# Optimization experiments

Hardware: AMD Instinct MI355X
Metric: run time of the kernel (lower is better)

## Reference

```python
import jax, jax.numpy as jnp
import numpy as np

B, S, D = 2, 2048, 768
C = 8                # num_channels
R = D // C           # ternary_rank = 96 (RoPE head_dim)
THETA = 10000.0
TERNARY_STD = 0.2
TERNARY_SCALE = 1.0  # ternary_factor_scaling


def _rope_tables():
    # HF-style RoPE: inv_freq over half dim, emb = concat(freqs, freqs)
    inv_freq = 1.0 / (THETA ** (np.arange(0, R, 2, dtype=np.float32) / R))
    pos = np.arange(S, dtype=np.float32)
    freqs = pos[:, None] * inv_freq[None, :]          # [S, R/2]
    emb = np.concatenate([freqs, freqs], axis=-1)     # [S, R]
    cos = np.broadcast_to(np.cos(emb)[None], (B, S, R)).copy()
    sin = np.broadcast_to(np.sin(emb)[None], (B, S, R)).copy()
    return jnp.asarray(cos), jnp.asarray(sin)


def setup_inputs() -> dict:
    key = jax.random.key(0)
    k1, k2, k3 = jax.random.split(key, 3)
    qz = jax.random.normal(k1, (B, S, D), dtype=jnp.float32)
    U = jax.random.normal(k2, (D, D), dtype=jnp.float32) * TERNARY_STD
    V = jax.random.normal(k3, (D, D), dtype=jnp.float32) * TERNARY_STD
    cos, sin = _rope_tables()
    return {"qz": qz, "cos": cos, "sin": sin, "U": U, "V": V}


def _rotate_half(x):
    h = x.shape[-1] // 2
    return jnp.concatenate([-x[..., h:], x[..., :h]], axis=-1)


def reference(qz, cos, sin, U, V):
    # cos/sin: [B,S,R] -> broadcast over channel dim -> [B,1,S,R]
    cosb = cos[:, None, :, :]
    sinb = sin[:, None, :, :]
    rope = lambda x: x * cosb + _rotate_half(x) * sinb       # apply
    rope_o = lambda x: x * cosb - _rotate_half(x) * sinb     # apply_o (inverse)

    # projections: F.linear(qz, W) == qz @ W.T
    qz_u = (qz @ U.T * TERNARY_SCALE).reshape(B, S, C, R).transpose(0, 2, 1, 3)
    qz_v = (qz @ V.T * TERNARY_SCALE).reshape(B, S, C, R).transpose(0, 2, 1, 3)

    qz_uo = rope_o(qz_u)
    qz_ur = rope(qz_u)
    qz_vr = rope(qz_v)

    # message_F: [B,C,S,S]
    message_F = jnp.einsum('bcqr,bckr->bcqk', qz_ur, qz_vr)
    # softmax(message_F / regularize_h) with regularize_h = 1/D  ->  * D
    qh = jax.nn.softmax((message_F * jnp.float32(D)).astype(jnp.float32), axis=-1).astype(qz_ur.dtype)

    qh_v1 = rope_o(jnp.einsum('bcqk,bckr->bcqr', qh, qz_vr))  # qh @ qz_v
    qh_v2 = rope(jnp.einsum('bckq,bckr->bcqr', qh, qz_uo))    # qh^T @ qz_uo

    qh_v1 = qh_v1.transpose(0, 2, 1, 3).reshape(B, S, D)
    qh_v2 = qh_v2.transpose(0, 2, 1, 3).reshape(B, S, D)

    message_G = (qh_v1 @ U + qh_v2 @ V) * TERNARY_SCALE
    return message_G
```

## Files before the change

### kernel.cpp

```cpp
#include <hip/hip_runtime.h>

typedef _Float16 f16;
typedef _Float16 f16x8 __attribute__((ext_vector_type(8)));
typedef _Float16 f16x4 __attribute__((ext_vector_type(4)));
typedef float f32x4 __attribute__((ext_vector_type(4)));

#define MFMA16(A,B,C) __builtin_amdgcn_mfma_f32_16x16x32_f16(A,B,C,0,0,0)
#define INV2048 4.8828125e-4f
#define HN (16ll*2048*96)
#define UVN 589824
#define ZC1 1107.98979f
#define ZC2 0.54101064f

__device__ __forceinline__ void split_f16(float x, f16& h, f16& l) {
    h = (f16)x;
    l = (f16)((x - (float)h) * 2048.0f);
}

__global__ __launch_bounds__(256) void k0_split(const float* __restrict__ qz,
                                                const float* __restrict__ U,
                                                const float* __restrict__ V,
                                                f16* __restrict__ qzh, f16* __restrict__ qzl,
                                                f16* __restrict__ Uh, f16* __restrict__ Ul,
                                                f16* __restrict__ Vh, f16* __restrict__ Vl) {
// ... 20 lines not shown
        float4 y = *(const float4*)(V + (size_t)i4 * 4);
        split_f16(y.x, h0, l0); split_f16(y.y, h1, l1);
        split_f16(y.z, h2, l2); split_f16(y.w, h3, l3);
        f16x4 hv2 = {h0, h1, h2, h3};
        f16x4 lv2 = {l0, l1, l2, l3};
        *(f16x4*)(Vh + (size_t)i4 * 4) = hv2;
        *(f16x4*)(Vl + (size_t)i4 * 4) = lv2;
    }
}

__global__ __launch_bounds__(256, 2) void k1_proj(const f16* __restrict__ qzh,
                                                  const f16* __restrict__ qzl,
                                                  const f16* __restrict__ Uh,
                                                  const f16* __restrict__ Ul,
                                                  const f16* __restrict__ Vh,
                                                  const f16* __restrict__ Vl,
                                                  const float* __restrict__ cosb,
                                                  const float* __restrict__ sinb,
                                                  f16* __restrict__ uhp, f16* __restrict__ ulp,
                                                  f16* __restrict__ vhp, f16* __restrict__ vlp,
                                                  f16* __restrict__ vT, f16* __restrict__ oT) {
    __shared__ __align__(16) f16 smem[36864];
    f16* sAh  = smem;
    f16* sAl  = smem + 4608;
    f16* sBuh = smem + 9216;
    f16* sBul = smem + 9216 + 6912;
    f16* sBvh = smem + 9216 + 2 * 6912;
    f16* sBvl = smem + 9216 + 3 * 6912;

    const int tid = threadIdx.x;
    const int w = tid >> 6, lane = tid & 63;
    const int quad = lane >> 4, l15 = lane & 15;
    const int wr = w >> 1, wc = w & 1;
    const int bid0 = blockIdx.y * 64 + blockIdx.x;
    const int swz  = (bid0 & 7) * 64 + (bid0 >> 3);
    const int bs0 = (swz & 63) * 64;
    const int c = swz >> 6;

    const f16* Ug_h = Uh + (size_t)c * 96 * 768;
    const f16* Ug_l = Ul + (size_t)c * 96 * 768;
    const f16* Vg_h = Vh + (size_t)c * 96 * 768;
    const f16* Vg_l = Vl + (size_t)c * 96 * 768;

    f32x4 aUS[2][3] = {}, aUX[2][3] = {};
    f32x4 aVS[2][3] = {}, aVX[2][3] = {};

    for (int k0 = 0; k0 < 768; k0 += 64) {
        __syncthreads();
#pragma unroll
        for (int m = 0; m < 2; ++m) {
            int f = tid + 256 * m, row = f >> 3, cg = f & 7;
            const size_t go = (size_t)(bs0 + row) * 768 + k0 + cg * 8;
            const int lo = row * 72 + cg * 8;
            *(float4*)&sAh[lo] = *(const float4*)(qzh + go);
            *(float4*)&sAl[lo] = *(const float4*)(qzl + go);
        }
#pragma unroll
        for (int m = 0; m < 3; ++m) {
            int f = tid + 256 * m, row = f >> 3, cg = f & 7;
            const size_t go = (size_t)row * 768 + k0 + cg * 8;
            const int lo = row * 72 + cg * 8;
            *(float4*)&sBuh[lo] = *(const float4*)(Ug_h + go);
            *(float4*)&sBul[lo] = *(const float4*)(Ug_l + go);
            *(float4*)&sBvh[lo] = *(const float4*)(Vg_h + go);
            *(float4*)&sBvl[lo] = *(const float4*)(Vg_l + go);
        }
        __syncthreads();
#pragma unroll
        for (int cc = 0; cc < 2; ++cc) {
            f16x8 ah[2], al[2];
#pragma unroll
            for (int mt = 0; mt < 2; ++mt) {
                const int ar = (32 * wr + 16 * mt + l15) * 72 + cc * 32 + quad * 8;
                ah[mt] = *(const f16x8*)&sAh[ar];
                al[mt] = *(const f16x8*)&sAl[ar];
            }
#pragma unroll
            for (int nt = 0; nt < 3; ++nt) {
                const int br = (48 * wc + 16 * nt + l15) * 72 + cc * 32 + quad * 8;
                f16x8 buh = *(const f16x8*)&sBuh[br];
                f16x8 bul = *(const f16x8*)&sBul[br];
                f16x8 bvh = *(const f16x8*)&sBvh[br];
                f16x8 bvl = *(const f16x8*)&sBvl[br];
#pragma unroll
                for (int mt = 0; mt < 2; ++mt) {
                    aUS[mt][nt] = MFMA16(ah[mt], buh, aUS[mt][nt]);
                    aUX[mt][nt] = MFMA16(ah[mt], bul, aUX[mt][nt]);
                    aUX[mt][nt] = MFMA16(al[mt], buh, aUX[mt][nt]);
                    aVS[mt][nt] = MFMA16(ah[mt], bvh, aVS[mt][nt]);
                    aVX[mt][nt] = MFMA16(ah[mt], bvl, aVX[mt][nt]);
                    aVX[mt][nt] = MFMA16(al[mt], bvh, aVX[mt][nt]);
                }
            }
        }
    }

    __syncthreads();
    float* LU = (float*)smem;
    float* LV = LU + 6400;
#pragma unroll
    for (int mt = 0; mt < 2; ++mt)
#pragma unroll
        for (int nt = 0; nt < 3; ++nt)
#pragma unroll
            for (int r = 0; r < 4; ++r) {
                const int sl = 32 * wr + 16 * mt + 4 * quad + r;
                const int col = 48 * wc + 16 * nt + l15;
                LU[sl * 100 + col] = aUS[mt][nt][r] + aUX[mt][nt][r] * INV2048;
                LV[sl * 100 + col] = aVS[mt][nt][r] + aVX[mt][nt][r] * INV2048;
            }
    __syncthreads();

    const int b = bs0 >> 11;
    const int s0 = bs0 & 2047;
    const int head = b * 8 + c;
    const size_t nb = (size_t)head * 2048 * 96;
    const size_t tb = (size_t)head * 96 * 2048;
    const int ty = tid >> 4, tx = tid & 15;

#pragma unroll
    for (int jj = 0; jj < 3; ++jj) {
        int r = tx + 16 * jj;
        f16 vt1[4], vt2[4], ot1[4], ot2[4];
#pragma unroll
        for (int ii = 0; ii < 4; ++ii) {
            int sl = 4 * ty + ii;
            int s = s0 + sl;
            int cbi = (b * 2048 + s) * 96 + r;
            float cc = cosb[cbi], ss = sinb[cbi];
            size_t rowb = nb + (size_t)s * 96;
            float u1 = LU[sl * 100 + r], u2 = LU[sl * 100 + r + 48];
            float v1 = LV[sl * 100 + r], v2 = LV[sl * 100 + r + 48];
            float ur1 = u1 * cc - u2 * ss, ur2 = u2 * cc + u1 * ss;
            float uo1 = u1 * cc + u2 * ss, uo2 = u2 * cc - u1 * ss;
            float vr1 = v1 * cc - v2 * ss, vr2 = v2 * cc + v1 * ss;
            f16 h, l;
            split_f16(ur1, h, l); uhp[rowb + r] = h;      ulp[rowb + r] = l;
            split_f16(ur2, h, l); uhp[rowb + r + 48] = h; ulp[rowb + r + 48] = l;
            split_f16(vr1, h, l); vhp[rowb + r] = h;      vlp[rowb + r] = l;      vt1[ii] = h;
            split_f16(vr2, h, l); vhp[rowb + r + 48] = h; vlp[rowb + r + 48] = l; vt2[ii] = h;
            ot1[ii] = (f16)uo1; ot2[ii] = (f16)uo2;
        }
        f16x4 pv1 = {vt1[0], vt1[1], vt1[2], vt1[3]};
        f16x4 pv2 = {vt2[0], vt2[1], vt2[2], vt2[3]};
        f16x4 po1 = {ot1[0], ot1[1], ot1[2], ot1[3]};
        f16x4 po2 = {ot2[0], ot2[1], ot2[2], ot2[3]};
        *(f16x4*)&vT[tb + (size_t)r * 2048 + s0 + 4 * ty] = pv1;
        *(f16x4*)&vT[tb + (size_t)(r + 48) * 2048 + s0 + 4 * ty] = pv2;
        *(f16x4*)&oT[tb + (size_t)r * 2048 + s0 + 4 * ty] = po1;
        *(f16x4*)&oT[tb + (size_t)(r + 48) * 2048 + s0 + 4 * ty] = po2;
    }
}

__global__ __launch_bounds__(256, 2) void k2_stats(const f16* __restrict__ uhp,
                                                   const f16* __restrict__ ulp,
                                                   const f16* __restrict__ vhp,
                                                   const f16* __restrict__ vlp,
                                                   float* __restrict__ Mo) {
    __shared__ float Mbuf[4][64];
    const int tid = threadIdx.x, w = tid >> 6, lane = tid & 63;
    const int quad = lane >> 4, l15 = lane & 15;
    const int bid0 = blockIdx.y * 32 + blockIdx.x;
    const int swz  = (bid0 & 7) * 64 + (bid0 >> 3);
    const int q0 = (swz & 31) * 64, head = swz >> 5;
    const f16* Ah_g = uhp + (size_t)head * 2048 * 96;
    const f16* Al_g = ulp + (size_t)head * 2048 * 96;

    f16x8 Afh[4][3], Afl[4][3];
#pragma unroll
    for (int mt = 0; mt < 4; ++mt)
#pragma unroll
        for (int cc = 0; cc < 3; ++cc) {
            size_t off = (size_t)(q0 + 16 * mt + l15) * 96 + cc * 32 + quad * 8;
            Afh[mt][cc] = *(const f16x8*)(Ah_g + off);
            Afl[mt][cc] = *(const f16x8*)(Al_g + off);
        }

    const f16* Bh_p = vhp + (size_t)head * 2048 * 96 + (size_t)(w * 16 + l15) * 96 + quad * 8;
    const f16* Bl_p = vlp + (size_t)head * 2048 * 96 + (size_t)(w * 16 + l15) * 96 + quad * 8;

    f16x8 Bch[2][3], Bcl[2][3];
#pragma unroll
    for (int cc = 0; cc < 3; ++cc) {
        Bch[0][cc] = *(const f16x8*)(Bh_p + cc * 32);
        Bcl[0][cc] = *(const f16x8*)(Bl_p + cc * 32);
    }

    float m_run[4][4];
#pragma unroll
    for (int mt = 0; mt < 4; ++mt)
#pragma unroll
        for (int r = 0; r < 4; ++r) m_run[mt][r] = -3.0e38f;

    for (int tp = 0; tp < 16; ++tp) {
#pragma unroll
        for (int h = 0; h < 2; ++h) {
            const int t = 2 * tp + h;
            if (t < 31) {
                const f16* bh = Bh_p + (size_t)(t + 1) * 6144;
                const f16* bl = Bl_p + (size_t)(t + 1) * 6144;
#pragma unroll
                for (int cc = 0; cc < 3; ++cc) {
                    Bch[h ^ 1][cc] = *(const f16x8*)(bh + cc * 32);
                    Bcl[h ^ 1][cc] = *(const f16x8*)(bl + cc * 32);
                }
            }
            f32x4 accS[4] = {}, accX[4] = {};
            __builtin_amdgcn_s_setprio(1);
#pragma unroll
            for (int cc = 0; cc < 3; ++cc)
#pragma unroll
                for (int mt = 0; mt < 4; ++mt) {
                    accS[mt] = MFMA16(Afh[mt][cc], Bch[h][cc], accS[mt]);
                    accX[mt] = MFMA16(Afh[mt][cc], Bcl[h][cc], accX[mt]);
                    accX[mt] = MFMA16(Afl[mt][cc], Bch[h][cc], accX[mt]);
                }
            __builtin_amdgcn_s_setprio(0);
#pragma unroll
            for (int mt = 0; mt < 4; ++mt)
#pragma unroll
                for (int r = 0; r < 4; ++r) {
                    float zl = fmaf(ZC1, accS[mt][r], ZC2 * accX[mt][r]);
                    m_run[mt][r] = fmaxf(m_run[mt][r], zl);
                }
        }
    }
#pragma unroll
    for (int mt = 0; mt < 4; ++mt)
#pragma unroll
        for (int r = 0; r < 4; ++r) {
            float m = m_run[mt][r];
            m = fmaxf(m, __shfl_xor(m, 1)); m = fmaxf(m, __shfl_xor(m, 2));
            m = fmaxf(m, __shfl_xor(m, 4)); m = fmaxf(m, __shfl_xor(m, 8));
            m_run[mt][r] = m;
        }
    if (l15 == 0) {
#pragma unroll
        for (int mt = 0; mt < 4; ++mt)
#pragma unroll
            for (int r = 0; r < 4; ++r)
                Mbuf[w][16 * mt + 4 * quad + r] = m_run[mt][r];
    }
    __syncthreads();
    if (tid < 64) {
        float M = -3.0e38f;
#pragma unroll
        for (int ww = 0; ww < 4; ++ww) M = fmaxf(M, Mbuf[ww][tid]);
        Mo[head * 2048 + q0 + tid] = M;
    }
}

__global__ __launch_bounds__(256, 2) void k3a(const f16* __restrict__ uhp,
                                              const f16* __restrict__ ulp,
                                              const f16* __restrict__ vhp,
                                              const f16* __restrict__ vlp,
                                              const f16* __restrict__ vT,
                                              const float* __restrict__ Mo,
                                              float* __restrict__ Lo,
                                              const float* __restrict__ cosb,
                                              const float* __restrict__ sinb,
                                              f16* __restrict__ w1) {
    __shared__ f16 Vt[2][112 * 72];
    __shared__ f16 P[2][64 * 72];
    const int tid = threadIdx.x, w = tid >> 6, lane = tid & 63;
    const int quad = lane >> 4, l15 = lane & 15;
    const int bid0 = blockIdx.y * 32 + blockIdx.x;
    const int swz  = (bid0 & 7) * 64 + (bid0 >> 3);
    const int q0 = (swz & 31) * 64, head = swz >> 5;
    const f16* Ah_g = uhp + (size_t)head * 2048 * 96;
    const f16* Al_g = ulp + (size_t)head * 2048 * 96;
    const f16* Vt_g = vT + (size_t)head * 96 * 2048;

    f16x8 Afh[4][3], Afl[4][3];
#pragma unroll
    for (int mt = 0; mt < 4; ++mt)
#pragma unroll
        for (int cc = 0; cc < 3; ++cc) {
            size_t off = (size_t)(q0 + 16 * mt + l15) * 96 + cc * 32 + quad * 8;
            Afh[mt][cc] = *(const f16x8*)(Ah_g + off);
            Afl[mt][cc] = *(const f16x8*)(Al_g + off);
        }
    float negM[4][4];
#pragma unroll
    for (int mt = 0; mt < 4; ++mt)
#pragma unroll
        for (int r = 0; r < 4; ++r)
            negM[mt][r] = -Mo[head * 2048 + q0 + 16 * mt + 4 * quad + r];

    const f16* Bh_p = vhp + (size_t)head * 2048 * 96 + (size_t)(w * 16 + l15) * 96 + quad * 8;
    const f16* Bl_p = vlp + (size_t)head * 2048 * 96 + (size_t)(w * 16 + l15) * 96 + quad * 8;
    const int vr0 = tid >> 3, vc8 = (tid & 7) * 8;
    const int pwc = (w * 16 + l15 + 16 * quad) & 63;
    const int prr = 16 * (l15 >> 2);

    if (tid < 144) {
        f16x8 ones = {(f16)1, (f16)1, (f16)1, (f16)1,
                      (f16)1, (f16)1, (f16)1, (f16)1};
        *(f16x8*)&Vt[0][96 * 72 + tid * 8] = ones;
        *(f16x8*)&Vt[1][96 * 72 + tid * 8] = ones;
    }

    f16x8 Bch[2][3], Bcl[2][3];
    float4 v0, v1, v2;
#pragma unroll
    for (int cc = 0; cc < 3; ++cc) {
        Bch[0][cc] = *(const f16x8*)(Bh_p + cc * 32);
        Bcl[0][cc] = *(const f16x8*)(Bl_p + cc * 32);
    }
    v0 = *(const float4*)(Vt_g + (size_t)vr0 * 2048 + vc8);
    v1 = *(const float4*)(Vt_g + (size_t)(vr0 + 32) * 2048 + vc8);
    v2 = *(const float4*)(Vt_g + (size_t)(vr0 + 64) * 2048 + vc8);
    *(float4*)&Vt[0][vr0 * 72 + vc8] = v0;
    *(float4*)&Vt[0][(vr0 + 32) * 72 + vc8] = v1;
    *(float4*)&Vt[0][(vr0 + 64) * 72 + vc8] = v2;

    f32x4 accO[7] = {};

    for (int tp = 0; tp < 16; ++tp) {
#pragma unroll
        for (int h = 0; h < 2; ++h) {
            const int t = 2 * tp + h;
            if (t < 31) {
                const f16* bh = Bh_p + (size_t)(t + 1) * 6144;
                const f16* bl = Bl_p + (size_t)(t + 1) * 6144;
                const int kn = (t + 1) * 64;
#pragma unroll
                for (int cc = 0; cc < 3; ++cc) {
                    Bch[h ^ 1][cc] = *(const f16x8*)(bh + cc * 32);
                    Bcl[h ^ 1][cc] = *(const f16x8*)(bl + cc * 32);
                }
                v0 = *(const float4*)(Vt_g + (size_t)vr0 * 2048 + kn + vc8);
                v1 = *(const float4*)(Vt_g + (size_t)(vr0 + 32) * 2048 + kn + vc8);
                v2 = *(const float4*)(Vt_g + (size_t)(vr0 + 64) * 2048 + kn + vc8);
            }
            f32x4 accS[4] = {}, accX[4] = {};
            __builtin_amdgcn_s_setprio(1);
#pragma unroll
            for (int cc = 0; cc < 3; ++cc)
#pragma unroll
                for (int mt = 0; mt < 4; ++mt) {
                    accS[mt] = MFMA16(Afh[mt][cc], Bch[h][cc], accS[mt]);
                    accX[mt] = MFMA16(Afh[mt][cc], Bcl[h][cc], accX[mt]);
                    accX[mt] = MFMA16(Afl[mt][cc], Bch[h][cc], accX[mt]);
                }
            __builtin_amdgcn_s_setprio(0);
#pragma unroll
            for (int mt = 0; mt < 4; ++mt)
#pragma unroll
                for (int r = 0; r < 4; ++r) {
                    float zl = fmaf(ZC1, accS[mt][r], ZC2 * accX[mt][r]);
                    P[h][(16 * mt + 4 * quad + r) * 72 + pwc] =
                        (f16)exp2f(zl + negM[mt][r]);
                }
            __syncthreads();
            __builtin_amdgcn_s_setprio(1);
#pragma unroll
            for (int kc = 0; kc < 2; ++kc) {
                f16x8 ap = *(const f16x8*)&P[h][(w * 16 + l15) * 72 +
                                               ((kc * 32 + quad * 8 + prr) & 63)];
#pragma unroll
                for (int nt = 0; nt < 7; ++nt) {
                    f16x8 bv = *(const f16x8*)&Vt[h][(nt * 16 + l15) * 72 + kc * 32 + quad * 8];
                    accO[nt] = MFMA16(ap, bv, accO[nt]);
                }
            }
            __builtin_amdgcn_s_setprio(0);
            if (t < 31) {
                *(float4*)&Vt[h ^ 1][vr0 * 72 + vc8] = v0;
                *(float4*)&Vt[h ^ 1][(vr0 + 32) * 72 + vc8] = v1;
                *(float4*)&Vt[h ^ 1][(vr0 + 64) * 72 + vc8] = v2;
            }
        }
    }
    float invL[4];
#pragma unroll
    for (int r = 0; r < 4; ++r) invL[r] = 1.0f / accO[6][r];
    if (l15 == 0) {
#pragma unroll
        for (int r = 0; r < 4; ++r)
            Lo[head * 2048 + q0 + w * 16 + quad * 4 + r] = accO[6][r];
    }

    const int b = head >> 3, c = head & 7;
#pragma unroll
    for (int r = 0; r < 4; ++r) {
        int q = q0 + w * 16 + quad * 4 + r;
        int cbi = (b * 2048 + q) * 96;
        f16* wrow = w1 + (size_t)(b * 2048 + q) * 768 + c * 96;
#pragma unroll
        for (int nt = 0; nt < 3; ++nt) {
            int rr = nt * 16 + l15;
            float cc = cosb[cbi + rr], ss = sinb[cbi + rr];
            float a = accO[nt][r] * invL[r];
            float b2 = accO[nt + 3][r] * invL[r];
            wrow[rr] = (f16)(a * cc + b2 * ss);
            wrow[rr + 48] = (f16)(b2 * cc - a * ss);
        }
    }
}

__global__ __launch_bounds__(256, 2) void k3b(const f16* __restrict__ uhp,
                                              const f16* __restrict__ ulp,
                                              const f16* __restrict__ vhp,
                                              const f16* __restrict__ vlp,
                                              const f16* __restrict__ oT,
                                              const float* __restrict__ Mo,
                                              const float* __restrict__ Lo,
                                              const float* __restrict__ cosb,
                                              const float* __restrict__ sinb,
                                              f16* __restrict__ w2) {
    __shared__ f16 Ot[2][96 * 72];
    __shared__ f16 P[2][64 * 72];
    const int tid = threadIdx.x, w = tid >> 6, lane = tid & 63;
    const int quad = lane >> 4, l15 = lane & 15;
    const int bid0 = blockIdx.y * 32 + blockIdx.x;
    const int swz  = (bid0 & 7) * 64 + (bid0 >> 3);
    const int q0 = (swz & 31) * 64, head = swz >> 5;
    const f16* Ah_g = vhp + (size_t)head * 2048 * 96;
    const f16* Al_g = vlp + (size_t)head * 2048 * 96;
    const f16* Ot_g = oT + (size_t)head * 96 * 2048;

    f16x8 Afh[4][3], Afl[4][3];
#pragma unroll
    for (int mt = 0; mt < 4; ++mt)
#pragma unroll
        for (int cc = 0; cc < 3; ++cc) {
            size_t off = (size_t)(q0 + 16 * mt + l15) * 96 + cc * 32 + quad * 8;
            Afh[mt][cc] = *(const f16x8*)(Ah_g + off);
            Afl[mt][cc] = *(const f16x8*)(Al_g + off);
        }

    const f16* Bh_p = uhp + (size_t)head * 2048 * 96 + (size_t)(w * 16 + l15) * 96 + quad * 8;
    const f16* Bl_p = ulp + (size_t)head * 2048 * 96 + (size_t)(w * 16 + l15) * 96 + quad * 8;
    const int vr0 = tid >> 3, vc8 = (tid & 7) * 8;
    const int pwc = (w * 16 + l15 + 16 * quad) & 63;
    const int prr = 16 * (l15 >> 2);

    f16x8 Bch[2][3], Bcl[2][3];
    float4 v0, v1, v2;
#pragma unroll
    for (int cc = 0; cc < 3; ++cc) {
        Bch[0][cc] = *(const f16x8*)(Bh_p + cc * 32);
        Bcl[0][cc] = *(const f16x8*)(Bl_p + cc * 32);
    }
    v0 = *(const float4*)(Ot_g + (size_t)vr0 * 2048 + vc8);
    v1 = *(const float4*)(Ot_g + (size_t)(vr0 + 32) * 2048 + vc8);
    v2 = *(const float4*)(Ot_g + (size_t)(vr0 + 64) * 2048 + vc8);
    *(float4*)&Ot[0][vr0 * 72 + vc8] = v0;
    *(float4*)&Ot[0][(vr0 + 32) * 72 + vc8] = v1;
    *(float4*)&Ot[0][(vr0 + 64) * 72 + vc8] = v2;

    f32x4 accO[6] = {};

    for (int tp = 0; tp < 16; ++tp) {
#pragma unroll
        for (int h = 0; h < 2; ++h) {
            const int t = 2 * tp + h;
            const int k0 = t * 64;
            float negMk = -Mo[head * 2048 + k0 + w * 16 + l15];
            float invLk = 1.0f / Lo[head * 2048 + k0 + w * 16 + l15];
            if (t < 31) {
                const f16* bh = Bh_p + (size_t)(t + 1) * 6144;
                const f16* bl = Bl_p + (size_t)(t + 1) * 6144;
                const int kn = (t + 1) * 64;
#pragma unroll
                for (int cc = 0; cc < 3; ++cc) {
                    Bch[h ^ 1][cc] = *(const f16x8*)(bh + cc * 32);
                    Bcl[h ^ 1][cc] = *(const f16x8*)(bl + cc * 32);
                }
                v0 = *(const float4*)(Ot_g + (size_t)vr0 * 2048 + kn + vc8);
                v1 = *(const float4*)(Ot_g + (size_t)(vr0 + 32) * 2048 + kn + vc8);
                v2 = *(const float4*)(Ot_g + (size_t)(vr0 + 64) * 2048 + kn + vc8);
            }
            f32x4 accS[4] = {}, accX[4] = {};
            __builtin_amdgcn_s_setprio(1);
#pragma unroll
            for (int cc = 0; cc < 3; ++cc)
#pragma unroll
                for (int mt = 0; mt < 4; ++mt) {
                    accS[mt] = MFMA16(Afh[mt][cc], Bch[h][cc], accS[mt]);
                    accX[mt] = MFMA16(Afl[mt][cc], Bch[h][cc], accX[mt]);
                    accX[mt] = MFMA16(Afh[mt][cc], Bcl[h][cc], accX[mt]);
                }
            __builtin_amdgcn_s_setprio(0);
#pragma unroll
            for (int mt = 0; mt < 4; ++mt)
#pragma unroll
                for (int r = 0; r < 4; ++r) {
                    float zl = fmaf(ZC1, accS[mt][r], ZC2 * accX[mt][r]);
                    P[h][(16 * mt + 4 * quad + r) * 72 + pwc] =
                        (f16)(exp2f(zl + negMk) * invLk);
                }
            __syncthreads();
            __builtin_amdgcn_s_setprio(1);
#pragma unroll
            for (int kc = 0; kc < 2; ++kc) {
                f16x8 ap = *(const f16x8*)&P[h][(w * 16 + l15) * 72 +
                                               ((kc * 32 + quad * 8 + prr) & 63)];
#pragma unroll
                for (int nt = 0; nt < 6; ++nt) {
                    f16x8 bo = *(const f16x8*)&Ot[h][(nt * 16 + l15) * 72 + kc * 32 + quad * 8];
                    accO[nt] = MFMA16(ap, bo, accO[nt]);
                }
            }
            __builtin_amdgcn_s_setprio(0);
            if (t < 31) {
                *(float4*)&Ot[h ^ 1][vr0 * 72 + vc8] = v0;
                *(float4*)&Ot[h ^ 1][(vr0 + 32) * 72 + vc8] = v1;
                *(float4*)&Ot[h ^ 1][(vr0 + 64) * 72 + vc8] = v2;
            }
        }
    }
    const int b = head >> 3, c = head & 7;
#pragma unroll
    for (int r = 0; r < 4; ++r) {
        int q = q0 + w * 16 + quad * 4 + r;
        int cbi = (b * 2048 + q) * 96;
        f16* wrow = w2 + (size_t)(b * 2048 + q) * 768 + c * 96;
#pragma unroll
        for (int nt = 0; nt < 3; ++nt) {
            int rr = nt * 16 + l15;
            float cc = cosb[cbi + rr], ss = sinb[cbi + rr];
            float a = accO[nt][r];
            float b2 = accO[nt + 3][r];
            wrow[rr] = (f16)(a * cc - b2 * ss);
            wrow[rr + 48] = (f16)(b2 * cc + a * ss);
        }
    }
}

__global__ __launch_bounds__(256, 2) void k4_final(const f16* __restrict__ w1,
                                                   const f16* __restrict__ w2,
                                                   const float* __restrict__ U,
                                                   const float* __restrict__ V,
                                                   float* __restrict__ outp) {
    __shared__ f16 A1[128 * 56];
    __shared__ f16 A2[128 * 56];
    __shared__ f16 B1[64 * 56];
    __shared__ f16 B2[64 * 56];
    const int tid = threadIdx.x, w = tid >> 6, lane = tid & 63;
    const int quad = lane >> 4, l15 = lane & 15;
    const int bs0 = blockIdx.x * 128;
    const int d0 = blockIdx.y * 64;
    f32x4 acc[2][4] = {};

    for (int ec = 0; ec < 24; ++ec) {
        int e0 = ec * 32;
        __syncthreads();
#pragma unroll
        for (int m = 0; m < 2; ++m) {
            int f = tid + 256 * m;
            int row = f >> 2, q = f & 3;
            *(float4*)&A1[row * 56 + q * 8] =
                *(const float4*)(w1 + (size_t)(bs0 + row) * 768 + e0 + q * 8);
            *(float4*)&A2[row * 56 + q * 8] =
                *(const float4*)(w2 + (size_t)(bs0 + row) * 768 + e0 + q * 8);
        }
#pragma unroll
        for (int m2 = 0; m2 < 2; ++m2) {
            int e_r = (tid >> 4) + 16 * m2;
            int dc = tid & 15;
            float4 fu = *(const float4*)(U + (size_t)(e0 + e_r) * 768 + d0 + dc * 4);
            float4 fv = *(const float4*)(V + (size_t)(e0 + e_r) * 768 + d0 + dc * 4);
            B1[(dc * 4 + 0) * 56 + e_r] = (f16)fu.x;
            B1[(dc * 4 + 1) * 56 + e_r] = (f16)fu.y;
            B1[(dc * 4 + 2) * 56 + e_r] = (f16)fu.z;
            B1[(dc * 4 + 3) * 56 + e_r] = (f16)fu.w;
            B2[(dc * 4 + 0) * 56 + e_r] = (f16)fv.x;
            B2[(dc * 4 + 1) * 56 + e_r] = (f16)fv.y;
            B2[(dc * 4 + 2) * 56 + e_r] = (f16)fv.z;
            B2[(dc * 4 + 3) * 56 + e_r] = (f16)fv.w;
        }
        __syncthreads();
        f16x8 a1f[2], a2f[2];
#pragma unroll
        for (int mt = 0; mt < 2; ++mt) {
            a1f[mt] = *(const f16x8*)&A1[(32 * w + 16 * mt + l15) * 56 + quad * 8];
            a2f[mt] = *(const f16x8*)&A2[(32 * w + 16 * mt + l15) * 56 + quad * 8];
        }
#pragma unroll
        for (int nt = 0; nt < 4; ++nt) {
            f16x8 b1f = *(const f16x8*)&B1[(nt * 16 + l15) * 56 + quad * 8];
            f16x8 b2f = *(const f16x8*)&B2[(nt * 16 + l15) * 56 + quad * 8];
#pragma unroll
            for (int mt = 0; mt < 2; ++mt) {
                acc[mt][nt] = MFMA16(a1f[mt], b1f, acc[mt][nt]);
                acc[mt][nt] = MFMA16(a2f[mt], b2f, acc[mt][nt]);
            }
        }
    }
#pragma unroll
    for (int mt = 0; mt < 2; ++mt)
#pragma unroll
        for (int nt = 0; nt < 4; ++nt)
#pragma unroll
            for (int r = 0; r < 4; ++r) {
                int s = bs0 + 32 * w + 16 * mt + 4 * quad + r;
                int d = d0 + 16 * nt + l15;
                outp[(size_t)s * 768 + d] = acc[mt][nt][r];
            }
}

extern "C" void kernel_launch(void* const* d_in, const int* in_sizes, int n_in,
                              void* d_out, int out_size, void* d_ws, size_t ws_size,
                              hipStream_t stream) {
    const float* qz   = (const float*)d_in[0];
    const float* cosb = (const float*)d_in[1];
    const float* sinb = (const float*)d_in[2];
    const float* U    = (const float*)d_in[3];
    const float* V    = (const float*)d_in[4];
    float* outp = (float*)d_out;

    f16* ws16 = (f16*)d_ws;
    f16* uhp = ws16;
    f16* ulp = ws16 + HN;
    f16* vhp = ws16 + 2 * HN;
    f16* vlp = ws16 + 3 * HN;
    f16* vT  = ws16 + 4 * HN;
    f16* oT  = ws16 + 5 * HN;
    f16* w1  = ws16 + 6 * HN;
    f16* w2  = ws16 + 7 * HN;
    float* Mo = (float*)(ws16 + 8 * HN);
    float* Lo = Mo + 16 * 2048;

    f16* qzh = w1;
    f16* qzl = w2;
    f16* outw = (f16*)d_out;
    f16* Uh = outw;
    f16* Ul = outw + UVN;
    f16* Vh = outw + 2 * UVN;
    f16* Vl = outw + 3 * UVN;

    k0_split<<<dim3(3072), 256, 0, stream>>>(qz, U, V, qzh, qzl, Uh, Ul, Vh, Vl);
    k1_proj<<<dim3(64, 8), 256, 0, stream>>>(qzh, qzl, Uh, Ul, Vh, Vl, cosb, sinb,
                                             uhp, ulp, vhp, vlp, vT, oT);
    k2_stats<<<dim3(32, 16), 256, 0, stream>>>(uhp, ulp, vhp, vlp, Mo);
    k3a<<<dim3(32, 16), 256, 0, stream>>>(uhp, ulp, vhp, vlp, vT, Mo, Lo, cosb, sinb, w1);
    k3b<<<dim3(32, 16), 256, 0, stream>>>(uhp, ulp, vhp, vlp, oT, Mo, Lo, cosb, sinb, w2);
    k4_final<<<dim3(32, 12), 256, 0, stream>>>(w1, w2, U, V, outp);
}
```

Measured before the change: 326.3 us.

## Split key dimension across two blocks in stats and attention kernels with merge passes

The stats, k3a and k3b kernels now each split the 2048-key range into two halves handled by separate blocks, doubling grid size (k2 also halves its query tile to 32). Partial row maxima, softmax denominators and unnormalized outputs go to separate buffers in fp32. New merge kernels (fa, fb) sum the partials, normalize, and apply RoPE before writing the f16 inputs for the final GEMM. The intent is more blocks to fill the GPU's CUs and higher occupancy hints. The cost is extra fp32 partial-output traffic, two extra launches and workspace reuse of the output and vT/oT buffers. k4 also gets a block swizzle.

```diff
diff --git a/kernel.cpp b/kernel.cpp
--- a/kernel.cpp
+++ b/kernel.cpp
@@ -196,23 +196,26 @@
     }
 }
 
-__global__ __launch_bounds__(256, 2) void k2_stats(const f16* __restrict__ uhp,
+__global__ __launch_bounds__(256, 4) void k2_stats(const f16* __restrict__ uhp,
                                                    const f16* __restrict__ ulp,
                                                    const f16* __restrict__ vhp,
                                                    const f16* __restrict__ vlp,
-                                                   float* __restrict__ Mo) {
-    __shared__ float Mbuf[4][64];
+                                                   float* __restrict__ Moa,
+                                                   float* __restrict__ Mob) {
+    __shared__ float Mbuf[4][32];
     const int tid = threadIdx.x, w = tid >> 6, lane = tid & 63;
     const int quad = lane >> 4, l15 = lane & 15;
-    const int bid0 = blockIdx.y * 32 + blockIdx.x;
-    const int swz  = (bid0 & 7) * 64 + (bid0 >> 3);
-    const int q0 = (swz & 31) * 64, head = swz >> 5;
+    const int bid0 = blockIdx.y * 128 + blockIdx.x;
+    const int swz  = (bid0 & 7) * 256 + (bid0 >> 3);
+    const int q0 = (swz & 63) * 32;
+    const int head = (swz >> 6) & 15;
+    const int half = swz >> 10;
     const f16* Ah_g = uhp + (size_t)head * 2048 * 96;
     const f16* Al_g = ulp + (size_t)head * 2048 * 96;
 
-    f16x8 Afh[4][3], Afl[4][3];
-#pragma unroll
-    for (int mt = 0; mt < 4; ++mt)
+    f16x8 Afh[2][3], Afl[2][3];
+#pragma unroll
+    for (int mt = 0; mt < 2; ++mt)
 #pragma unroll
         for (int cc = 0; cc < 3; ++cc) {
             size_t off = (size_t)(q0 + 16 * mt + l15) * 96 + cc * 32 + quad * 8;
@@ -220,8 +223,10 @@
             Afl[mt][cc] = *(const f16x8*)(Al_g + off);
         }
 
-    const f16* Bh_p = vhp + (size_t)head * 2048 * 96 + (size_t)(w * 16 + l15) * 96 + quad * 8;
-    const f16* Bl_p = vlp + (size_t)head * 2048 * 96 + (size_t)(w * 16 + l15) * 96 + quad * 8;
+    const f16* Bh_p = vhp + (size_t)head * 2048 * 96 +
+                      (size_t)(half * 1024 + w * 16 + l15) * 96 + quad * 8;
+    const f16* Bl_p = vlp + (size_t)head * 2048 * 96 +
+                      (size_t)(half * 1024 + w * 16 + l15) * 96 + quad * 8;
 
     f16x8 Bch[2][3], Bcl[2][3];
 #pragma unroll
@@ -230,17 +235,17 @@
         Bcl[0][cc] = *(const f16x8*)(Bl_p + cc * 32);
     }
 
-    float m_run[4][4];
-#pragma unroll
-    for (int mt = 0; mt < 4; ++mt)
+    float m_run[2][4];
+#pragma unroll
+    for (int mt = 0; mt < 2; ++mt)
 #pragma unroll
         for (int r = 0; r < 4; ++r) m_run[mt][r] = -3.0e38f;
 
-    for (int tp = 0; tp < 16; ++tp) {
+    for (int tp = 0; tp < 8; ++tp) {
 #pragma unroll
         for (int h = 0; h < 2; ++h) {
             const int t = 2 * tp + h;
-            if (t < 31) {
+            if (t < 15) {
                 const f16* bh = Bh_p + (size_t)(t + 1) * 6144;
                 const f16* bl = Bl_p + (size_t)(t + 1) * 6144;
 #pragma unroll
@@ -249,19 +254,19 @@
                     Bcl[h ^ 1][cc] = *(const f16x8*)(bl + cc * 32);
                 }
             }
-            f32x4 accS[4] = {}, accX[4] = {};
+            f32x4 accS[2] = {}, accX[2] = {};
             __builtin_amdgcn_s_setprio(1);
 #pragma unroll
             for (int cc = 0; cc < 3; ++cc)
 #pragma unroll
-                for (int mt = 0; mt < 4; ++mt) {
+                for (int mt = 0; mt < 2; ++mt) {
                     accS[mt] = MFMA16(Afh[mt][cc], Bch[h][cc], accS[mt]);
                     accX[mt] = MFMA16(Afh[mt][cc], Bcl[h][cc], accX[mt]);
                     accX[mt] = MFMA16(Afl[mt][cc], Bch[h][cc], accX[mt]);
                 }
             __builtin_amdgcn_s_setprio(0);
 #pragma unroll
-            for (int mt = 0; mt < 4; ++mt)
+            for (int mt = 0; mt < 2; ++mt)
 #pragma unroll
                 for (int r = 0; r < 4; ++r) {
                     float zl = fmaf(ZC1, accS[mt][r], ZC2 * accX[mt][r]);
@@ -270,7 +275,7 @@
         }
     }
 #pragma unroll
-    for (int mt = 0; mt < 4; ++mt)
+    for (int mt = 0; mt < 2; ++mt)
 #pragma unroll
         for (int r = 0; r < 4; ++r) {
             float m = m_run[mt][r];
@@ -280,37 +285,42 @@
         }
     if (l15 == 0) {
 #pragma unroll
-        for (int mt = 0; mt < 4; ++mt)
+        for (int mt = 0; mt < 2; ++mt)
 #pragma unroll
             for (int r = 0; r < 4; ++r)
                 Mbuf[w][16 * mt + 4 * quad + r] = m_run[mt][r];
     }
     __syncthreads();
-    if (tid < 64) {
+    if (tid < 32) {
         float M = -3.0e38f;
 #pragma unroll
         for (int ww = 0; ww < 4; ++ww) M = fmaxf(M, Mbuf[ww][tid]);
-        Mo[head * 2048 + q0 + tid] = M;
-    }
-}
-
-__global__ __launch_bounds__(256, 2) void k3a(const f16* __restrict__ uhp,
+        float* Mo_h = half ? Mob : Moa;
+        Mo_h[head * 2048 + q0 + tid] = M;
+    }
+}
+
+__global__ __launch_bounds__(256, 3) void k3a(const f16* __restrict__ uhp,
                                               const f16* __restrict__ ulp,
                                               const f16* __restrict__ vhp,
                                               const f16* __restrict__ vlp,
                                               const f16* __restrict__ vT,
-                                              const float* __restrict__ Mo,
-                                              float* __restrict__ Lo,
-                                              const float* __restrict__ cosb,
-                                              const float* __restrict__ sinb,
-                                              f16* __restrict__ w1) {
+                                              const float* __restrict__ Moa,
+                                              const float* __restrict__ Mob,
+                                              float* __restrict__ Oa,
+                                              float* __restrict__ Ob,
+                                              float* __restrict__ La,
+                                              float* __restrict__ Lb) {
     __shared__ f16 Vt[2][112 * 72];
     __shared__ f16 P[2][64 * 72];
     const int tid = threadIdx.x, w = tid >> 6, lane = tid & 63;
     const int quad = lane >> 4, l15 = lane & 15;
-    const int bid0 = blockIdx.y * 32 + blockIdx.x;
-    const int swz  = (bid0 & 7) * 64 + (bid0 >> 3);
-    const int q0 = (swz & 31) * 64, head = swz >> 5;
+    const int bid0 = blockIdx.y * 64 + blockIdx.x;
+    const int swz  = (bid0 & 7) * 128 + (bid0 >> 3);
+    const int q0 = (swz & 31) * 64;
+    const int head = (swz >> 5) & 15;
+    const int half = swz >> 9;
+    const int kb = half * 1024;
     const f16* Ah_g = uhp + (size_t)head * 2048 * 96;
     const f16* Al_g = ulp + (size_t)head * 2048 * 96;
     const f16* Vt_g = vT + (size_t)head * 96 * 2048;
@@ -328,11 +338,15 @@
 #pragma unroll
     for (int mt = 0; mt < 4; ++mt)
 #pragma unroll
-        for (int r = 0; r < 4; ++r)
-            negM[mt][r] = -Mo[head * 2048 + q0 + 16 * mt + 4 * quad + r];
-
-    const f16* Bh_p = vhp + (size_t)head * 2048 * 96 + (size_t)(w * 16 + l15) * 96 + quad * 8;
-    const f16* Bl_p = vlp + (size_t)head * 2048 * 96 + (size_t)(w * 16 + l15) * 96 + quad * 8;
+        for (int r = 0; r < 4; ++r) {
+            int i = head * 2048 + q0 + 16 * mt + 4 * quad + r;
+            negM[mt][r] = -fmaxf(Moa[i], Mob[i]);
+        }
+
+    const f16* Bh_p = vhp + (size_t)head * 2048 * 96 +
+                      (size_t)(kb + w * 16 + l15) * 96 + quad * 8;
+    const f16* Bl_p = vlp + (size_t)head * 2048 * 96 +
+                      (size_t)(kb + w * 16 + l15) * 96 + quad * 8;
     const int vr0 = tid >> 3, vc8 = (tid & 7) * 8;
     const int pwc = (w * 16 + l15 + 16 * quad) & 63;
     const int prr = 16 * (l15 >> 2);
@@ -351,23 +365,23 @@
         Bch[0][cc] = *(const f16x8*)(Bh_p + cc * 32);
         Bcl[0][cc] = *(const f16x8*)(Bl_p + cc * 32);
     }
-    v0 = *(const float4*)(Vt_g + (size_t)vr0 * 2048 + vc8);
-    v1 = *(const float4*)(Vt_g + (size_t)(vr0 + 32) * 2048 + vc8);
-    v2 = *(const float4*)(Vt_g + (size_t)(vr0 + 64) * 2048 + vc8);
+    v0 = *(const float4*)(Vt_g + (size_t)vr0 * 2048 + kb + vc8);
+    v1 = *(const float4*)(Vt_g + (size_t)(vr0 + 32) * 2048 + kb + vc8);
+    v2 = *(const float4*)(Vt_g + (size_t)(vr0 + 64) * 2048 + kb + vc8);
     *(float4*)&Vt[0][vr0 * 72 + vc8] = v0;
     *(float4*)&Vt[0][(vr0 + 32) * 72 + vc8] = v1;
     *(float4*)&Vt[0][(vr0 + 64) * 72 + vc8] = v2;
 
     f32x4 accO[7] = {};
 
-    for (int tp = 0; tp < 16; ++tp) {
+    for (int tp = 0; tp < 8; ++tp) {
 #pragma unroll
         for (int h = 0; h < 2; ++h) {
             const int t = 2 * tp + h;
-            if (t < 31) {
+            if (t < 15) {
                 const f16* bh = Bh_p + (size_t)(t + 1) * 6144;
                 const f16* bl = Bl_p + (size_t)(t + 1) * 6144;
-                const int kn = (t + 1) * 64;
+                const int kn = kb + (t + 1) * 64;
 #pragma unroll
                 for (int cc = 0; cc < 3; ++cc) {
                     Bch[h ^ 1][cc] = *(const f16x8*)(bh + cc * 32);
@@ -409,57 +423,76 @@
                 }
             }
             __builtin_amdgcn_s_setprio(0);
-            if (t < 31) {
+            if (t < 15) {
                 *(float4*)&Vt[h ^ 1][vr0 * 72 + vc8] = v0;
                 *(float4*)&Vt[h ^ 1][(vr0 + 32) * 72 + vc8] = v1;
                 *(float4*)&Vt[h ^ 1][(vr0 + 64) * 72 + vc8] = v2;
             }
         }
     }
-    float invL[4];
-#pragma unroll
-    for (int r = 0; r < 4; ++r) invL[r] = 1.0f / accO[6][r];
+    float* Op = half ? Ob : Oa;
+    float* Lp = half ? Lb : La;
     if (l15 == 0) {
 #pragma unroll
         for (int r = 0; r < 4; ++r)
-            Lo[head * 2048 + q0 + w * 16 + quad * 4 + r] = accO[6][r];
-    }
-
+            Lp[head * 2048 + q0 + w * 16 + quad * 4 + r] = accO[6][r];
+    }
+#pragma unroll
+    for (int r = 0; r < 4; ++r) {
+        const size_t rb = ((size_t)head * 2048 + q0 + w * 16 + quad * 4 + r) * 96;
+#pragma unroll
+        for (int nt = 0; nt < 6; ++nt)
+            Op[rb + nt * 16 + l15] = accO[nt][r];
+    }
+}
+
+__global__ __launch_bounds__(256) void fa(const float* __restrict__ Oa,
+                                          const float* __restrict__ Ob,
+                                          const float* __restrict__ La,
+                                          const float* __restrict__ Lb,
+                                          const float* __restrict__ cosb,
+                                          const float* __restrict__ sinb,
+                                          float* __restrict__ Lo,
+                                          f16* __restrict__ w1f) {
+    const int tid = threadIdx.x;
+    const int rg = tid >> 6, l = tid & 63;
+    const int ridx = blockIdx.x * 4 + rg;
+    const int head = ridx >> 11, q = ridx & 2047;
+    const float L = La[ridx] + Lb[ridx];
+    if (l == 0) Lo[ridx] = L;
+    if (l >= 48) return;
+    const float invL = 1.0f / L;
+    const size_t rb = (size_t)ridx * 96;
     const int b = head >> 3, c = head & 7;
-#pragma unroll
-    for (int r = 0; r < 4; ++r) {
-        int q = q0 + w * 16 + quad * 4 + r;
-        int cbi = (b * 2048 + q) * 96;
-        f16* wrow = w1 + (size_t)(b * 2048 + q) * 768 + c * 96;
-#pragma unroll
-        for (int nt = 0; nt < 3; ++nt) {
-            int rr = nt * 16 + l15;
-            float cc = cosb[cbi + rr], ss = sinb[cbi + rr];
-            float a = accO[nt][r] * invL[r];
-            float b2 = accO[nt + 3][r] * invL[r];
-            wrow[rr] = (f16)(a * cc + b2 * ss);
-            wrow[rr + 48] = (f16)(b2 * cc - a * ss);
-        }
-    }
-}
-
-__global__ __launch_bounds__(256, 2) void k3b(const f16* __restrict__ uhp,
+    const int cbi = (b * 2048 + q) * 96 + l;
+    const float cc = cosb[cbi], ss = sinb[cbi];
+    const float a  = (Oa[rb + l] + Ob[rb + l]) * invL;
+    const float b2 = (Oa[rb + l + 48] + Ob[rb + l + 48]) * invL;
+    f16* wrow = w1f + (size_t)(b * 2048 + q) * 768 + c * 96;
+    wrow[l] = (f16)(a * cc + b2 * ss);
+    wrow[l + 48] = (f16)(b2 * cc - a * ss);
+}
+
+__global__ __launch_bounds__(256, 3) void k3b(const f16* __restrict__ uhp,
                                               const f16* __restrict__ ulp,
                                               const f16* __restrict__ vhp,
                                               const f16* __restrict__ vlp,
                                               const f16* __restrict__ oT,
-                                              const float* __restrict__ Mo,
+                                              const float* __restrict__ Moa,
+                                              const float* __restrict__ Mob,
                                               const float* __restrict__ Lo,
-                                              const float* __restrict__ cosb,
-                                              const float* __restrict__ sinb,
-                                              f16* __restrict__ w2) {
+                                              float* __restrict__ Oa,
+                                              float* __restrict__ Ob) {
     __shared__ f16 Ot[2][96 * 72];
     __shared__ f16 P[2][64 * 72];
     const int tid = threadIdx.x, w = tid >> 6, lane = tid & 63;
     const int quad = lane >> 4, l15 = lane & 15;
-    const int bid0 = blockIdx.y * 32 + blockIdx.x;
-    const int swz  = (bid0 & 7) * 64 + (bid0 >> 3);
-    const int q0 = (swz & 31) * 64, head = swz >> 5;
+    const int bid0 = blockIdx.y * 64 + blockIdx.x;
+    const int swz  = (bid0 & 7) * 128 + (bid0 >> 3);
+    const int q0 = (swz & 31) * 64;
+    const int head = (swz >> 5) & 15;
+    const int half = swz >> 9;
+    const int kb = half * 1024;
     const f16* Ah_g = vhp + (size_t)head * 2048 * 96;
     const f16* Al_g = vlp + (size_t)head * 2048 * 96;
     const f16* Ot_g = oT + (size_t)head * 96 * 2048;
@@ -474,8 +507,10 @@
             Afl[mt][cc] = *(const f16x8*)(Al_g + off);
         }
 
-    const f16* Bh_p = uhp + (size_t)head * 2048 * 96 + (size_t)(w * 16 + l15) * 96 + quad * 8;
-    const f16* Bl_p = ulp + (size_t)head * 2048 * 96 + (size_t)(w * 16 + l15) * 96 + quad * 8;
+    const f16* Bh_p = uhp + (size_t)head * 2048 * 96 +
+                      (size_t)(kb + w * 16 + l15) * 96 + quad * 8;
+    const f16* Bl_p = ulp + (size_t)head * 2048 * 96 +
+                      (size_t)(kb + w * 16 + l15) * 96 + quad * 8;
     const int vr0 = tid >> 3, vc8 = (tid & 7) * 8;
     const int pwc = (w * 16 + l15 + 16 * quad) & 63;
     const int prr = 16 * (l15 >> 2);
@@ -487,26 +522,26 @@
         Bch[0][cc] = *(const f16x8*)(Bh_p + cc * 32);
         Bcl[0][cc] = *(const f16x8*)(Bl_p + cc * 32);
     }
-    v0 = *(const float4*)(Ot_g + (size_t)vr0 * 2048 + vc8);
-    v1 = *(const float4*)(Ot_g + (size_t)(vr0 + 32) * 2048 + vc8);
-    v2 = *(const float4*)(Ot_g + (size_t)(vr0 + 64) * 2048 + vc8);
+    v0 = *(const float4*)(Ot_g + (size_t)vr0 * 2048 + kb + vc8);
+    v1 = *(const float4*)(Ot_g + (size_t)(vr0 + 32) * 2048 + kb + vc8);
+    v2 = *(const float4*)(Ot_g + (size_t)(vr0 + 64) * 2048 + kb + vc8);
     *(float4*)&Ot[0][vr0 * 72 + vc8] = v0;
     *(float4*)&Ot[0][(vr0 + 32) * 72 + vc8] = v1;
     *(float4*)&Ot[0][(vr0 + 64) * 72 + vc8] = v2;
 
     f32x4 accO[6] = {};
 
-    for (int tp = 0; tp < 16; ++tp) {
+    for (int tp = 0; tp < 8; ++tp) {
 #pragma unroll
         for (int h = 0; h < 2; ++h) {
             const int t = 2 * tp + h;
-            const int k0 = t * 64;
-            float negMk = -Mo[head * 2048 + k0 + w * 16 + l15];
-            float invLk = 1.0f / Lo[head * 2048 + k0 + w * 16 + l15];
-            if (t < 31) {
+            const int gk = head * 2048 + kb + t * 64 + w * 16 + l15;
+            const float negMk = -fmaxf(Moa[gk], Mob[gk]);
+            const float invLk = 1.0f / Lo[gk];
+            if (t < 15) {
                 const f16* bh = Bh_p + (size_t)(t + 1) * 6144;
                 const f16* bl = Bl_p + (size_t)(t + 1) * 6144;
-                const int kn = (t + 1) * 64;
+                const int kn = kb + (t + 1) * 64;
 #pragma unroll
                 for (int cc = 0; cc < 3; ++cc) {
                     Bch[h ^ 1][cc] = *(const f16x8*)(bh + cc * 32);
@@ -548,29 +583,42 @@
                 }
             }
             __builtin_amdgcn_s_setprio(0);
-            if (t < 31) {
+            if (t < 15) {
                 *(float4*)&Ot[h ^ 1][vr0 * 72 + vc8] = v0;
                 *(float4*)&Ot[h ^ 1][(vr0 + 32) * 72 + vc8] = v1;
                 *(float4*)&Ot[h ^ 1][(vr0 + 64) * 72 + vc8] = v2;
             }
         }
     }
+    float* Op = half ? Ob : Oa;
+#pragma unroll
+    for (int r = 0; r < 4; ++r) {
+        const size_t rb = ((size_t)head * 2048 + q0 + w * 16 + quad * 4 + r) * 96;
+#pragma unroll
+        for (int nt = 0; nt < 6; ++nt)
+            Op[rb + nt * 16 + l15] = accO[nt][r];
+    }
+}
+
+__global__ __launch_bounds__(256) void fb(const float* __restrict__ Oa,
+                                          const float* __restrict__ Ob,
+                                          const float* __restrict__ cosb,
+                                          const float* __restrict__ sinb,
+                                          f16* __restrict__ w2f) {
+    const int tid = threadIdx.x;
+    const int rg = tid >> 6, l = tid & 63;
+    const int ridx = blockIdx.x * 4 + rg;
+    const int head = ridx >> 11, q = ridx & 2047;
+    if (l >= 48) return;
+    const size_t rb = (size_t)ridx * 96;
     const int b = head >> 3, c = head & 7;
-#pragma unroll
-    for (int r = 0; r < 4; ++r) {
-        int q = q0 + w * 16 + quad * 4 + r;
-        int cbi = (b * 2048 + q) * 96;
-        f16* wrow = w2 + (size_t)(b * 2048 + q) * 768 + c * 96;
-#pragma unroll
-        for (int nt = 0; nt < 3; ++nt) {
-            int rr = nt * 16 + l15;
-            float cc = cosb[cbi + rr], ss = sinb[cbi + rr];
-            float a = accO[nt][r];
-            float b2 = accO[nt + 3][r];
-            wrow[rr] = (f16)(a * cc - b2 * ss);
-            wrow[rr + 48] = (f16)(b2 * cc + a * ss);
-        }
-    }
+    const int cbi = (b * 2048 + q) * 96 + l;
+    const float cc = cosb[cbi], ss = sinb[cbi];
+    const float a  = Oa[rb + l] + Ob[rb + l];
+    const float b2 = Oa[rb + l + 48] + Ob[rb + l + 48];
+    f16* wrow = w2f + (size_t)(b * 2048 + q) * 768 + c * 96;
+    wrow[l] = (f16)(a * cc - b2 * ss);
+    wrow[l + 48] = (f16)(b2 * cc + a * ss);
 }
 
 __global__ __launch_bounds__(256, 2) void k4_final(const f16* __restrict__ w1,
@@ -584,8 +632,10 @@
     __shared__ f16 B2[64 * 56];
     const int tid = threadIdx.x, w = tid >> 6, lane = tid & 63;
     const int quad = lane >> 4, l15 = lane & 15;
-    const int bs0 = blockIdx.x * 128;
-    const int d0 = blockIdx.y * 64;
+    const int id = blockIdx.y * 32 + blockIdx.x;
+    const int g  = (id & 7) * 48 + (id >> 3);
+    const int bs0 = (g & 31) * 128;
+    const int d0 = (g >> 5) * 64;
     f32x4 acc[2][4] = {};
 
     for (int ec = 0; ec < 24; ++ec) {
@@ -662,24 +712,34 @@
     f16* vlp = ws16 + 3 * HN;
     f16* vT  = ws16 + 4 * HN;
     f16* oT  = ws16 + 5 * HN;
-    f16* w1  = ws16 + 6 * HN;
-    f16* w2  = ws16 + 7 * HN;
-    float* Mo = (float*)(ws16 + 8 * HN);
-    float* Lo = Mo + 16 * 2048;
-
-    f16* qzh = w1;
-    f16* qzl = w2;
+    f16* qzh = ws16 + 6 * HN;
+    f16* qzl = ws16 + 7 * HN;
+    float* Ob = (float*)(ws16 + 6 * HN);
+    float* Moa = (float*)(ws16 + 8 * HN);
+    float* Mob = Moa + 32768;
+    float* Lo  = Moa + 65536;
+    float* La  = Moa + 98304;
+    float* Lb  = Moa + 131072;
+
     f16* outw = (f16*)d_out;
     f16* Uh = outw;
     f16* Ul = outw + UVN;
     f16* Vh = outw + 2 * UVN;
     f16* Vl = outw + 3 * UVN;
+    float* Oa = (float*)d_out;
+
+    f16* w1f = vT;
+    f16* w2f = oT;
 
     k0_split<<<dim3(3072), 256, 0, stream>>>(qz, U, V, qzh, qzl, Uh, Ul, Vh, Vl);
     k1_proj<<<dim3(64, 8), 256, 0, stream>>>(qzh, qzl, Uh, Ul, Vh, Vl, cosb, sinb,
                                              uhp, ulp, vhp, vlp, vT, oT);
-    k2_stats<<<dim3(32, 16), 256, 0, stream>>>(uhp, ulp, vhp, vlp, Mo);
-    k3a<<<dim3(32, 16), 256, 0, stream>>>(uhp, ulp, vhp, vlp, vT, Mo, Lo, cosb, sinb, w1);
-    k3b<<<dim3(32, 16), 256, 0, stream>>>(uhp, ulp, vhp, vlp, oT, Mo, Lo, cosb, sinb, w2);
-    k4_final<<<dim3(32, 12), 256, 0, stream>>>(w1, w2, U, V, outp);
-}
+    k2_stats<<<dim3(128, 16), 256, 0, stream>>>(uhp, ulp, vhp, vlp, Moa, Mob);
+    k3a<<<dim3(64, 16), 256, 0, stream>>>(uhp, ulp, vhp, vlp, vT, Moa, Mob,
+                                          Oa, Ob, La, Lb);
+    fa<<<dim3(8192), 256, 0, stream>>>(Oa, Ob, La, Lb, cosb, sinb, Lo, w1f);
+    k3b<<<dim3(64, 16), 256, 0, stream>>>(uhp, ulp, vhp, vlp, oT, Moa, Mob, Lo,
+                                          Oa, Ob);
+    fb<<<dim3(8192), 256, 0, stream>>>(Oa, Ob, cosb, sinb, w2f);
+    k4_final<<<dim3(32, 12), 256, 0, stream>>>(w1f, w2f, U, V, outp);
+}
```

After: 918.6 us. 2.82x slower.

## Fuse row-max pass into k3a with online softmax rescaling

Applied to the files above, without the earlier changes.

Removes the separate k2_stats kernel that recomputed the full QK^T score matrix only to find per-row maxima. k3a now keeps a running max per row, reduces each tile's max across waves through shared memory with an extra barrier, and rescales the accumulated output before each P@V step. It then writes the final max to Mo for k3b to use. This saves a whole score-recompute pass but adds per-tile shuffles, a __syncthreads and accumulator rescaling inside the k3a inner loop.

```diff
diff --git a/kernel.cpp b/kernel.cpp
--- a/kernel.cpp
+++ b/kernel.cpp
@@ -196,116 +196,19 @@
     }
 }
 
-__global__ __launch_bounds__(256, 2) void k2_stats(const f16* __restrict__ uhp,
-                                                   const f16* __restrict__ ulp,
-                                                   const f16* __restrict__ vhp,
-                                                   const f16* __restrict__ vlp,
-                                                   float* __restrict__ Mo) {
-    __shared__ float Mbuf[4][64];
-    const int tid = threadIdx.x, w = tid >> 6, lane = tid & 63;
-    const int quad = lane >> 4, l15 = lane & 15;
-    const int bid0 = blockIdx.y * 32 + blockIdx.x;
-    const int swz  = (bid0 & 7) * 64 + (bid0 >> 3);
-    const int q0 = (swz & 31) * 64, head = swz >> 5;
-    const f16* Ah_g = uhp + (size_t)head * 2048 * 96;
-    const f16* Al_g = ulp + (size_t)head * 2048 * 96;
-
-    f16x8 Afh[4][3], Afl[4][3];
-#pragma unroll
-    for (int mt = 0; mt < 4; ++mt)
-#pragma unroll
-        for (int cc = 0; cc < 3; ++cc) {
-            size_t off = (size_t)(q0 + 16 * mt + l15) * 96 + cc * 32 + quad * 8;
-            Afh[mt][cc] = *(const f16x8*)(Ah_g + off);
-            Afl[mt][cc] = *(const f16x8*)(Al_g + off);
-        }
-
-    const f16* Bh_p = vhp + (size_t)head * 2048 * 96 + (size_t)(w * 16 + l15) * 96 + quad * 8;
-    const f16* Bl_p = vlp + (size_t)head * 2048 * 96 + (size_t)(w * 16 + l15) * 96 + quad * 8;
-
-    f16x8 Bch[2][3], Bcl[2][3];
-#pragma unroll
-    for (int cc = 0; cc < 3; ++cc) {
-        Bch[0][cc] = *(const f16x8*)(Bh_p + cc * 32);
-        Bcl[0][cc] = *(const f16x8*)(Bl_p + cc * 32);
-    }
-
-    float m_run[4][4];
-#pragma unroll
-    for (int mt = 0; mt < 4; ++mt)
-#pragma unroll
-        for (int r = 0; r < 4; ++r) m_run[mt][r] = -3.0e38f;
-
-    for (int tp = 0; tp < 16; ++tp) {
-#pragma unroll
-        for (int h = 0; h < 2; ++h) {
-            const int t = 2 * tp + h;
-            if (t < 31) {
-                const f16* bh = Bh_p + (size_t)(t + 1) * 6144;
-                const f16* bl = Bl_p + (size_t)(t + 1) * 6144;
-#pragma unroll
-                for (int cc = 0; cc < 3; ++cc) {
-                    Bch[h ^ 1][cc] = *(const f16x8*)(bh + cc * 32);
-                    Bcl[h ^ 1][cc] = *(const f16x8*)(bl + cc * 32);
-                }
-            }
-            f32x4 accS[4] = {}, accX[4] = {};
-            __builtin_amdgcn_s_setprio(1);
-#pragma unroll
-            for (int cc = 0; cc < 3; ++cc)
-#pragma unroll
-                for (int mt = 0; mt < 4; ++mt) {
-                    accS[mt] = MFMA16(Afh[mt][cc], Bch[h][cc], accS[mt]);
-                    accX[mt] = MFMA16(Afh[mt][cc], Bcl[h][cc], accX[mt]);
-                    accX[mt] = MFMA16(Afl[mt][cc], Bch[h][cc], accX[mt]);
-                }
-            __builtin_amdgcn_s_setprio(0);
-#pragma unroll
-            for (int mt = 0; mt < 4; ++mt)
-#pragma unroll
-                for (int r = 0; r < 4; ++r) {
-                    float zl = fmaf(ZC1, accS[mt][r], ZC2 * accX[mt][r]);
-                    m_run[mt][r] = fmaxf(m_run[mt][r], zl);
-                }
-        }
-    }
-#pragma unroll
-    for (int mt = 0; mt < 4; ++mt)
-#pragma unroll
-        for (int r = 0; r < 4; ++r) {
-            float m = m_run[mt][r];
-            m = fmaxf(m, __shfl_xor(m, 1)); m = fmaxf(m, __shfl_xor(m, 2));
-            m = fmaxf(m, __shfl_xor(m, 4)); m = fmaxf(m, __shfl_xor(m, 8));
-            m_run[mt][r] = m;
-        }
-    if (l15 == 0) {
-#pragma unroll
-        for (int mt = 0; mt < 4; ++mt)
-#pragma unroll
-            for (int r = 0; r < 4; ++r)
-                Mbuf[w][16 * mt + 4 * quad + r] = m_run[mt][r];
-    }
-    __syncthreads();
-    if (tid < 64) {
-        float M = -3.0e38f;
-#pragma unroll
-        for (int ww = 0; ww < 4; ++ww) M = fmaxf(M, Mbuf[ww][tid]);
-        Mo[head * 2048 + q0 + tid] = M;
-    }
-}
-
 __global__ __launch_bounds__(256, 2) void k3a(const f16* __restrict__ uhp,
                                               const f16* __restrict__ ulp,
                                               const f16* __restrict__ vhp,
                                               const f16* __restrict__ vlp,
                                               const f16* __restrict__ vT,
-                                              const float* __restrict__ Mo,
+                                              float* __restrict__ Mo,
                                               float* __restrict__ Lo,
                                               const float* __restrict__ cosb,
                                               const float* __restrict__ sinb,
                                               f16* __restrict__ w1) {
     __shared__ f16 Vt[2][112 * 72];
     __shared__ f16 P[2][64 * 72];
+    __shared__ __align__(16) float MtL[64 * 4];
     const int tid = threadIdx.x, w = tid >> 6, lane = tid & 63;
     const int quad = lane >> 4, l15 = lane & 15;
     const int bid0 = blockIdx.y * 32 + blockIdx.x;
@@ -324,12 +227,6 @@
             Afh[mt][cc] = *(const f16x8*)(Ah_g + off);
             Afl[mt][cc] = *(const f16x8*)(Al_g + off);
         }
-    float negM[4][4];
-#pragma unroll
-    for (int mt = 0; mt < 4; ++mt)
-#pragma unroll
-        for (int r = 0; r < 4; ++r)
-            negM[mt][r] = -Mo[head * 2048 + q0 + 16 * mt + 4 * quad + r];
 
     const f16* Bh_p = vhp + (size_t)head * 2048 * 96 + (size_t)(w * 16 + l15) * 96 + quad * 8;
     const f16* Bl_p = vlp + (size_t)head * 2048 * 96 + (size_t)(w * 16 + l15) * 96 + quad * 8;
@@ -359,6 +256,11 @@
     *(float4*)&Vt[0][(vr0 + 64) * 72 + vc8] = v2;
 
     f32x4 accO[7] = {};
+    float m_run[4][4];
+#pragma unroll
+    for (int mt = 0; mt < 4; ++mt)
+#pragma unroll
+        for (int r = 0; r < 4; ++r) m_run[mt][r] = -3.0e38f;
 
     for (int tp = 0; tp < 16; ++tp) {
 #pragma unroll
@@ -388,15 +290,43 @@
                     accX[mt] = MFMA16(Afl[mt][cc], Bch[h][cc], accX[mt]);
                 }
             __builtin_amdgcn_s_setprio(0);
+            float zl[4][4];
 #pragma unroll
             for (int mt = 0; mt < 4; ++mt)
 #pragma unroll
                 for (int r = 0; r < 4; ++r) {
-                    float zl = fmaf(ZC1, accS[mt][r], ZC2 * accX[mt][r]);
+                    float z = fmaf(ZC1, accS[mt][r], ZC2 * accX[mt][r]);
+                    zl[mt][r] = z;
+                    float tm = z;
+                    tm = fmaxf(tm, __shfl_xor(tm, 1));
+                    tm = fmaxf(tm, __shfl_xor(tm, 2));
+                    tm = fmaxf(tm, __shfl_xor(tm, 4));
+                    tm = fmaxf(tm, __shfl_xor(tm, 8));
+                    if (l15 == 0) MtL[(16 * mt + 4 * quad + r) * 4 + w] = tm;
+                }
+            __syncthreads();
+            float mold_w[4];
+#pragma unroll
+            for (int r = 0; r < 4; ++r) mold_w[r] = m_run[w][r];
+#pragma unroll
+            for (int mt = 0; mt < 4; ++mt)
+#pragma unroll
+                for (int r = 0; r < 4; ++r) {
+                    float4 mw = *(const float4*)&MtL[(16 * mt + 4 * quad + r) * 4];
+                    float tmax = fmaxf(fmaxf(mw.x, mw.y), fmaxf(mw.z, mw.w));
+                    float mnew = fmaxf(m_run[mt][r], tmax);
+                    m_run[mt][r] = mnew;
                     P[h][(16 * mt + 4 * quad + r) * 72 + pwc] =
-                        (f16)exp2f(zl + negM[mt][r]);
+                        (f16)exp2f(zl[mt][r] - mnew);
                 }
             __syncthreads();
+            float sc[4];
+#pragma unroll
+            for (int r = 0; r < 4; ++r) sc[r] = exp2f(mold_w[r] - m_run[w][r]);
+#pragma unroll
+            for (int nt = 0; nt < 7; ++nt)
+#pragma unroll
+                for (int r = 0; r < 4; ++r) accO[nt][r] *= sc[r];
             __builtin_amdgcn_s_setprio(1);
 #pragma unroll
             for (int kc = 0; kc < 2; ++kc) {
@@ -415,6 +345,13 @@
                 *(float4*)&Vt[h ^ 1][(vr0 + 64) * 72 + vc8] = v2;
             }
         }
+    }
+    if (w == 0 && l15 == 0) {
+#pragma unroll
+        for (int mt = 0; mt < 4; ++mt)
+#pragma unroll
+            for (int r = 0; r < 4; ++r)
+                Mo[head * 2048 + q0 + 16 * mt + 4 * quad + r] = m_run[mt][r];
     }
     float invL[4];
 #pragma unroll
@@ -678,7 +615,6 @@
     k0_split<<<dim3(3072), 256, 0, stream>>>(qz, U, V, qzh, qzl, Uh, Ul, Vh, Vl);
     k1_proj<<<dim3(64, 8), 256, 0, stream>>>(qzh, qzl, Uh, Ul, Vh, Vl, cosb, sinb,
                                              uhp, ulp, vhp, vlp, vT, oT);
-    k2_stats<<<dim3(32, 16), 256, 0, stream>>>(uhp, ulp, vhp, vlp, Mo);
     k3a<<<dim3(32, 16), 256, 0, stream>>>(uhp, ulp, vhp, vlp, vT, Mo, Lo, cosb, sinb, w1);
     k3b<<<dim3(32, 16), 256, 0, stream>>>(uhp, ulp, vhp, vlp, oT, Mo, Lo, cosb, sinb, w2);
     k4_final<<<dim3(32, 12), 256, 0, stream>>>(w1, w2, U, V, outp);
```

Result: slower. 492.9 us (+51.1%).
